# Kernel optimization log

Hardware: AMD Instinct MI355X
Metric: run time of the kernel (lower is better)

The kernel has to match this reference:

```python
import jax, jax.numpy as jnp
import numpy as np

N = 100000   # nodes (single ntype)
R = 3        # relations
E = 500000   # edges per relation
H = 4        # attention heads
F = 64       # out_feat per head
IN = 256     # in_feat
NEG_SLOPE = 0.2  # DGL GATConv default


def setup_inputs() -> dict:
    key = jax.random.key(0)
    ks = jax.random.split(key, 7)
    x = jax.random.normal(ks[0], (N, IN), jnp.float32)
    src = jax.random.randint(ks[1], (R, E), 0, N, dtype=jnp.int32)
    dst = jax.random.randint(ks[2], (R, E), 0, N, dtype=jnp.int32)
    W = jax.random.normal(ks[3], (R, IN, H * F), jnp.float32) / np.sqrt(IN).astype(np.float32)
    attn_l = jax.random.normal(ks[4], (R, H, F), jnp.float32) * 0.1
    attn_r = jax.random.normal(ks[5], (R, H, F), jnp.float32) * 0.1
    bias = jnp.zeros((R, H * F), jnp.float32)
    return {"x": x, "W": W, "attn_l": attn_l, "attn_r": attn_r, "bias": bias,
            "src": src, "dst": dst}


def _gat_relation(x, W_r, al_r, ar_r, b_r, src_r, dst_r):
    # projection: [N, H, F]
    z = (x @ W_r).reshape(N, H, F)
    # per-node attention logits: [N, H]
    el = jnp.sum(z * al_r, axis=-1)
    er = jnp.sum(z * ar_r, axis=-1)
    # edge scores: [E, H]
    e = jax.nn.leaky_relu(el[src_r] + er[dst_r], negative_slope=NEG_SLOPE)
    # segment softmax over incoming edges of each dst node
    m = jax.ops.segment_max(e, dst_r, num_segments=N)      # [N, H]
    ee = jnp.exp(e - m[dst_r])                              # [E, H]
    den = jax.ops.segment_sum(ee, dst_r, num_segments=N)   # [N, H]
    alpha = ee / den[dst_r]                                 # [E, H]
    # weighted scatter-aggregate: [N, H, F]
    rst = jax.ops.segment_sum(z[src_r] * alpha[:, :, None], dst_r, num_segments=N)
    return rst + b_r.reshape(1, H, F)


def reference(x, W, attn_l, attn_r, bias, src, dst):
    # HeteroGraphConv aggregates relations targeting the same ntype with 'sum'
    out = jnp.zeros((N, H, F), x.dtype)
    for r in range(R):
        out = out + _gat_relation(x, W[r], attn_l[r], attn_r[r], bias[r], src[r], dst[r])
    # RelGATConvLayer._apply: activation(h.view(-1, out_feat*num_heads)); dropout=0
    return jax.nn.elu(out.reshape(N, H * F))
```

## Files before the change

### kernel.cpp

```cpp
#include <hip/hip_runtime.h>
#include <hip/hip_bf16.h>


#define RN 100000
#define RE 500000
#define RH 4
#define RIN 256
#define RR 3
#define RHF 256
#define NE3 (RR * RE)
#define N3  (RR * RN)

typedef __attribute__((ext_vector_type(8))) short short8;
typedef __attribute__((ext_vector_type(4))) float f32x4;

static __device__ __forceinline__ float b2f(unsigned short u) {
  return __uint_as_float(((unsigned int)u) << 16);
}
static __device__ __forceinline__ unsigned short f2b(float f) {
  unsigned int u = __float_as_uint(f);
  u += 0x7FFF + ((u >> 16) & 1);
  return (unsigned short)(u >> 16);
}

__global__ __launch_bounds__(256) void rgat_convx(
    const float* __restrict__ x, unsigned short* __restrict__ xb) {
  const size_t i = ((size_t)blockIdx.x * 256 + threadIdx.x) * 4;
  if (i >= (size_t)RN * RIN) return;
  const float4 v = *(const float4*)(x + i);
  ushort4 o;
  o.x = f2b(v.x); o.y = f2b(v.y); o.z = f2b(v.z); o.w = f2b(v.w);
  *(ushort4*)(xb + i) = o;
}

__global__ __launch_bounds__(256) void rgat_convw(
    const float* __restrict__ W, unsigned short* __restrict__ wbt) {
  const int o = blockIdx.x * 256 + threadIdx.x;
  if (o >= RR * RIN * RHF) return;
  const int r = o / (RIN * RHF);
  const int rem = o - r * (RIN * RHF);
  const int n = rem >> 8;
  const int k = rem & 255;
  wbt[o] = f2b(W[r * (RIN * RHF) + k * RHF + n]);
}

__global__ __launch_bounds__(256) void rgat_gemm_bf16(
    const unsigned short* __restrict__ xb, const unsigned short* __restrict__ wbt,
    unsigned short* __restrict__ zb, const float* __restrict__ al,
    const float* __restrict__ ar, float* __restrict__ el,
    float* __restrict__ er) {
  __shared__ unsigned short As[128 * 32];
  __shared__ unsigned short Bs[128 * 32];
  const int tid = threadIdx.x;
  const int lane = tid & 63, wid = tid >> 6;
  const int wr = wid >> 1, wc = wid & 1;
  const int m0 = blockIdx.x * 128;
  const int n0 = blockIdx.y * 128;
  const int r  = blockIdx.z;

  f32x4 acc[4][4] = {};
  const unsigned short* Bbase = wbt + (size_t)r * (RIN * RHF);

  for (int k0 = 0; k0 < RIN; k0 += 32) {
#pragma unroll
    for (int i = 0; i < 2; ++i) {
      const int c = wid * 128 + i * 64 + lane;
      const int row = c >> 2, c4 = c & 3;
      const unsigned short* ga = xb + (size_t)(m0 + row) * RIN + k0 + c4 * 8;
      __builtin_amdgcn_global_load_lds(
          (const __attribute__((address_space(1))) void*)ga,
          (__attribute__((address_space(3))) void*)(As + (wid * 128 + i * 64) * 8),
          16, 0, 0);
      const unsigned short* gb = Bbase + (size_t)(n0 + row) * RIN + k0 + c4 * 8;
      __builtin_amdgcn_global_load_lds(
          (const __attribute__((address_space(1))) void*)gb,
          (__attribute__((address_space(3))) void*)(Bs + (wid * 128 + i * 64) * 8),
          16, 0, 0);
    }
    asm volatile("s_waitcnt vmcnt(0)" ::: "memory");
    __syncthreads();

    short8 af[4], bfr[4];
#pragma unroll
    for (int mi = 0; mi < 4; ++mi)
      af[mi] = *(const short8*)(As + ((wr * 64 + mi * 16 + (lane & 15)) * 32 + (lane >> 4) * 8));
#pragma unroll
    for (int ni = 0; ni < 4; ++ni)
      bfr[ni] = *(const short8*)(Bs + ((wc * 64 + ni * 16 + (lane & 15)) * 32 + (lane >> 4) * 8));
#pragma unroll
    for (int mi = 0; mi < 4; ++mi)
#pragma unroll
      for (int ni = 0; ni < 4; ++ni)
        acc[mi][ni] = __builtin_amdgcn_mfma_f32_16x16x32_bf16(af[mi], bfr[ni], acc[mi][ni], 0, 0, 0);
    __syncthreads();
  }

  const int head = blockIdx.y * 2 + wc;
  float alv[4], arv[4];
#pragma unroll
  for (int ni = 0; ni < 4; ++ni) {
    alv[ni] = al[r * RHF + head * 64 + ni * 16 + (lane & 15)];
    arv[ni] = ar[r * RHF + head * 64 + ni * 16 + (lane & 15)];
  }

  const int mbase = m0 + wr * 64;
#pragma unroll
  for (int mi = 0; mi < 4; ++mi) {
#pragma unroll
    for (int q = 0; q < 4; ++q) {
      const int m = mbase + mi * 16 + (lane >> 4) * 4 + q;
      float pl = 0.f, pr = 0.f;
#pragma unroll
      for (int ni = 0; ni < 4; ++ni) {
        pl += acc[mi][ni][q] * alv[ni];
        pr += acc[mi][ni][q] * arv[ni];
      }
#pragma unroll
      for (int off = 1; off < 16; off <<= 1) {
        pl += __shfl_xor(pl, off);
        pr += __shfl_xor(pr, off);
      }
      if (m < RN) {
        if ((lane & 15) == 0) {
          el[(size_t)(r * (size_t)RN + m) * RH + head] = pl;
          er[(size_t)(r * (size_t)RN + m) * RH + head] = pr;
        }
        unsigned short* zrow = zb + (size_t)r * ((size_t)RN * RHF) + (size_t)m * RHF
                               + n0 + wc * 64 + (lane & 15);
#pragma unroll
        for (int ni = 0; ni < 4; ++ni) zrow[ni * 16] = f2b(acc[mi][ni][q]);
      }
    }
  }
}

__global__ __launch_bounds__(256) void rgat_hist(
    const int* __restrict__ dst, int* __restrict__ deg) {
  const int i = blockIdx.x * 256 + threadIdx.x;
  if (i >= NE3) return;
  const int r = i / RE;
  atomicAdd(&deg[r * RN + dst[i]], 1);
}

__global__ __launch_bounds__(256) void rgat_scan1(
    const int* __restrict__ deg, int* __restrict__ offs, int* __restrict__ bsum) {
  __shared__ int sh[256];
  const int tid = threadIdx.x;
  const int base = blockIdx.x * 1024 + tid * 4;
  int v[4]; int s = 0;
#pragma unroll
  for (int j = 0; j < 4; ++j) {
    v[j] = (base + j < N3) ? deg[base + j] : 0;
    s += v[j];
  }
  sh[tid] = s;
  __syncthreads();
  for (int off = 1; off < 256; off <<= 1) {
    int t = (tid >= off) ? sh[tid - off] : 0;
    __syncthreads();
    sh[tid] += t;
    __syncthreads();
  }
  int run = sh[tid] - s;
  if (tid == 255) bsum[blockIdx.x] = sh[255];
#pragma unroll
  for (int j = 0; j < 4; ++j) {
    if (base + j < N3) offs[base + j] = run;
    run += v[j];
  }
}

__global__ __launch_bounds__(512) void rgat_scan2(int* __restrict__ bsum, int nb) {
  __shared__ int sh[512];
  const int tid = threadIdx.x;
  const int v = (tid < nb) ? bsum[tid] : 0;
  sh[tid] = v;
  __syncthreads();
  for (int off = 1; off < 512; off <<= 1) {
    int t = (tid >= off) ? sh[tid - off] : 0;
    __syncthreads();
    sh[tid] += t;
    __syncthreads();
  }
  if (tid < nb) bsum[tid] = sh[tid] - v;
}

__global__ __launch_bounds__(256) void rgat_scan3(
    int* __restrict__ offs, const int* __restrict__ bsum) {
  const int base = blockIdx.x * 1024 + threadIdx.x * 4;
  const int b = bsum[blockIdx.x];
#pragma unroll
  for (int j = 0; j < 4; ++j)
    if (base + j < N3) offs[base + j] += b;
}

__global__ __launch_bounds__(256) void rgat_scatter(
    const int* __restrict__ src, const int* __restrict__ dst,
    const float* __restrict__ el, const float* __restrict__ er,
    int* __restrict__ offs, int* __restrict__ csr_src,
    float4* __restrict__ csr_ee) {
  const int i = blockIdx.x * 256 + threadIdx.x;
  if (i >= NE3) return;
  const int r = i / RE;
  const int s = src[i];
  const int d = dst[i];
  const int pos = atomicAdd(&offs[r * RN + d], 1);
  const float4 elv = *(const float4*)(el + (size_t)(r * (size_t)RN + s) * RH);
  const float4 erv = *(const float4*)(er + (size_t)(r * (size_t)RN + d) * RH);
  float e0 = elv.x + erv.x, e1 = elv.y + erv.y, e2 = elv.z + erv.z, e3 = elv.w + erv.w;
  e0 = e0 > 0.f ? e0 : 0.2f * e0;
  e1 = e1 > 0.f ? e1 : 0.2f * e1;
  e2 = e2 > 0.f ? e2 : 0.2f * e2;
  e3 = e3 > 0.f ? e3 : 0.2f * e3;
  csr_src[pos] = s;
  csr_ee[pos] = make_float4(__expf(e0), __expf(e1), __expf(e2), __expf(e3));
}

__global__ __launch_bounds__(256) void rgat_aggregate(
    const unsigned short* __restrict__ zb, const int* __restrict__ csr_src,
    const float4* __restrict__ csr_ee, const int* __restrict__ deg,
    const int* __restrict__ offs, const float* __restrict__ bias,
    float* __restrict__ out) {
  __shared__ float sh[3][RHF];
  const int n = blockIdx.x;
  const int wid = threadIdx.x >> 6, lane = threadIdx.x & 63;
  const int h = lane >> 4;
  const int c = lane * 4;

  if (wid < 3) {
    const int r = wid;
    const int base = r * RN + n;
    const int d = deg[base];
    float a0 = 0.f, a1 = 0.f, a2 = 0.f, a3 = 0.f, den = 0.f;
    if (d > 0) {
      const int start = offs[base] - d;
      const unsigned short* zr = zb + (size_t)r * ((size_t)RN * RHF) + c;
      int s = csr_src[start];
      float4 ee = csr_ee[start];
      ushort4 zv = *(const ushort4*)(zr + (size_t)s * RHF);
      for (int e = 0; e < d; ++e) {
        const float a = (h == 0) ? ee.x : (h == 1) ? ee.y : (h == 2) ? ee.z : ee.w;
        const ushort4 zc = zv;
        if (e + 1 < d) {
          s = csr_src[start + e + 1];
          ee = csr_ee[start + e + 1];
          zv = *(const ushort4*)(zr + (size_t)s * RHF);
        }
        a0 += a * b2f(zc.x);
        a1 += a * b2f(zc.y);
        a2 += a * b2f(zc.z);
        a3 += a * b2f(zc.w);
        den += a;
      }
    }
    const float inv = (den > 0.f) ? 1.f / den : 0.f;
    *(float4*)&sh[r][c] = make_float4(a0 * inv, a1 * inv, a2 * inv, a3 * inv);
  }
  __syncthreads();

  const int col = threadIdx.x;
  float v = sh[0][col] + sh[1][col] + sh[2][col]
          + bias[col] + bias[RHF + col] + bias[2 * RHF + col];
  v = v > 0.f ? v : (__expf(v) - 1.f);
  out[(size_t)n * RHF + col] = v;
}

extern "C" void kernel_launch(void* const* d_in, const int* in_sizes, int n_in,
                              void* d_out, int out_size, void* d_ws, size_t ws_size,
                              hipStream_t stream) {
  const float* x    = (const float*)d_in[0];
  const float* W    = (const float*)d_in[1];
  const float* al   = (const float*)d_in[2];
  const float* ar   = (const float*)d_in[3];
  const float* bias = (const float*)d_in[4];
  const int*   src  = (const int*)d_in[5];
  const int*   dst  = (const int*)d_in[6];
  float* out = (float*)d_out;

  char* p = (char*)d_ws;
  unsigned short* xb  = (unsigned short*)p; p += (size_t)RN * RIN * 2;
  unsigned short* wbt = (unsigned short*)p; p += (size_t)RR * RIN * RHF * 2;
  unsigned short* zb  = (unsigned short*)p; p += (size_t)RR * RN * RHF * 2;
  float* el   = (float*)p;  p += (size_t)N3 * RH * 4;
  float* er   = (float*)p;  p += (size_t)N3 * RH * 4;
  int* deg    = (int*)p;    p += (size_t)N3 * 4;
  int* offs   = (int*)p;    p += (size_t)N3 * 4;
  int* csr_s  = (int*)p;    p += (size_t)NE3 * 4;
  float4* csr_ee = (float4*)p; p += (size_t)NE3 * 16;
  int* bsum   = (int*)p;    p += 2048;

  const int NB1 = (N3 + 1023) / 1024;

  hipMemsetAsync(deg, 0, (size_t)N3 * 4, stream);

  rgat_convx<<<(RN * RIN / 4 + 255) / 256, 256, 0, stream>>>(x, xb);
  rgat_convw<<<(RR * RIN * RHF + 255) / 256, 256, 0, stream>>>(W, wbt);

  rgat_hist<<<(NE3 + 255) / 256, 256, 0, stream>>>(dst, deg);
  rgat_scan1<<<NB1, 256, 0, stream>>>(deg, offs, bsum);
  rgat_scan2<<<1, 512, 0, stream>>>(bsum, NB1);
  rgat_scan3<<<NB1, 256, 0, stream>>>(offs, bsum);

  rgat_gemm_bf16<<<dim3((RN + 127) / 128, RHF / 128, RR), 256, 0, stream>>>(
      xb, wbt, zb, al, ar, el, er);

  rgat_scatter<<<(NE3 + 255) / 256, 256, 0, stream>>>(src, dst, el, er, offs,
                                                      csr_s, csr_ee);

  rgat_aggregate<<<RN, 256, 0, stream>>>(zb, csr_s, csr_ee, deg, offs, bias, out);
}
```

Measured before the change: 753.0 us.

## Merge relation CSRs by destination and split edges across all four warps

Builds one CSR keyed only by destination node, merging the three relations, and stores a combined relation-and-source row offset per edge. The aggregate kernel then spreads each node's edges over all four warps in batches of four independent gathers, instead of one warp per relation walking a serial dependent chain with the fourth warp idle. Each edge is routed to a per-relation accumulator by its offset range, and the partial sums and denominators are reduced in shared memory. This shrinks the histogram and scan to N entries and raises memory-level parallelism, at the cost of extra branching per edge and more shared-memory reduction work.

```diff
diff --git a/kernel.cpp b/kernel.cpp
--- a/kernel.cpp
+++ b/kernel.cpp
@@ -9,7 +9,6 @@
 #define RR 3
 #define RHF 256
 #define NE3 (RR * RE)
-#define N3  (RR * RN)
 
 typedef __attribute__((ext_vector_type(8))) short short8;
 typedef __attribute__((ext_vector_type(4))) float f32x4;
@@ -135,11 +134,10 @@
 }
 
 __global__ __launch_bounds__(256) void rgat_hist(
-    const int* __restrict__ dst, int* __restrict__ deg) {
+    const int* __restrict__ dst, int* __restrict__ degm) {
   const int i = blockIdx.x * 256 + threadIdx.x;
   if (i >= NE3) return;
-  const int r = i / RE;
-  atomicAdd(&deg[r * RN + dst[i]], 1);
+  atomicAdd(&degm[dst[i]], 1);
 }
 
 __global__ __launch_bounds__(256) void rgat_scan1(
@@ -150,7 +148,7 @@
   int v[4]; int s = 0;
 #pragma unroll
   for (int j = 0; j < 4; ++j) {
-    v[j] = (base + j < N3) ? deg[base + j] : 0;
+    v[j] = (base + j < RN) ? deg[base + j] : 0;
     s += v[j];
   }
   sh[tid] = s;
@@ -165,7 +163,7 @@
   if (tid == 255) bsum[blockIdx.x] = sh[255];
 #pragma unroll
   for (int j = 0; j < 4; ++j) {
-    if (base + j < N3) offs[base + j] = run;
+    if (base + j < RN) offs[base + j] = run;
     run += v[j];
   }
 }
@@ -191,20 +189,20 @@
   const int b = bsum[blockIdx.x];
 #pragma unroll
   for (int j = 0; j < 4; ++j)
-    if (base + j < N3) offs[base + j] += b;
+    if (base + j < RN) offs[base + j] += b;
 }
 
 __global__ __launch_bounds__(256) void rgat_scatter(
     const int* __restrict__ src, const int* __restrict__ dst,
     const float* __restrict__ el, const float* __restrict__ er,
-    int* __restrict__ offs, int* __restrict__ csr_src,
-    float4* __restrict__ csr_ee) {
+    int* __restrict__ offsm, int* __restrict__ czoff,
+    float4* __restrict__ cee) {
   const int i = blockIdx.x * 256 + threadIdx.x;
   if (i >= NE3) return;
   const int r = i / RE;
   const int s = src[i];
   const int d = dst[i];
-  const int pos = atomicAdd(&offs[r * RN + d], 1);
+  const int pos = atomicAdd(&offsm[d], 1);
   const float4 elv = *(const float4*)(el + (size_t)(r * (size_t)RN + s) * RH);
   const float4 erv = *(const float4*)(er + (size_t)(r * (size_t)RN + d) * RH);
   float e0 = elv.x + erv.x, e1 = elv.y + erv.y, e2 = elv.z + erv.z, e3 = elv.w + erv.w;
@@ -212,55 +210,81 @@
   e1 = e1 > 0.f ? e1 : 0.2f * e1;
   e2 = e2 > 0.f ? e2 : 0.2f * e2;
   e3 = e3 > 0.f ? e3 : 0.2f * e3;
-  csr_src[pos] = s;
-  csr_ee[pos] = make_float4(__expf(e0), __expf(e1), __expf(e2), __expf(e3));
+  czoff[pos] = r * RN + s;
+  cee[pos] = make_float4(__expf(e0), __expf(e1), __expf(e2), __expf(e3));
 }
 
 __global__ __launch_bounds__(256) void rgat_aggregate(
-    const unsigned short* __restrict__ zb, const int* __restrict__ csr_src,
-    const float4* __restrict__ csr_ee, const int* __restrict__ deg,
-    const int* __restrict__ offs, const float* __restrict__ bias,
+    const unsigned short* __restrict__ zb, const int* __restrict__ czoff,
+    const float4* __restrict__ cee, const int* __restrict__ degm,
+    const int* __restrict__ offsm, const float* __restrict__ bias,
     float* __restrict__ out) {
-  __shared__ float sh[3][RHF];
+  __shared__ float shn[4][RR][RHF];
+  __shared__ float shd[4][RR][RH];
   const int n = blockIdx.x;
   const int wid = threadIdx.x >> 6, lane = threadIdx.x & 63;
   const int h = lane >> 4;
   const int c = lane * 4;
 
-  if (wid < 3) {
-    const int r = wid;
-    const int base = r * RN + n;
-    const int d = deg[base];
-    float a0 = 0.f, a1 = 0.f, a2 = 0.f, a3 = 0.f, den = 0.f;
-    if (d > 0) {
-      const int start = offs[base] - d;
-      const unsigned short* zr = zb + (size_t)r * ((size_t)RN * RHF) + c;
-      int s = csr_src[start];
-      float4 ee = csr_ee[start];
-      ushort4 zv = *(const ushort4*)(zr + (size_t)s * RHF);
-      for (int e = 0; e < d; ++e) {
-        const float a = (h == 0) ? ee.x : (h == 1) ? ee.y : (h == 2) ? ee.z : ee.w;
-        const ushort4 zc = zv;
-        if (e + 1 < d) {
-          s = csr_src[start + e + 1];
-          ee = csr_ee[start + e + 1];
-          zv = *(const ushort4*)(zr + (size_t)s * RHF);
-        }
-        a0 += a * b2f(zc.x);
-        a1 += a * b2f(zc.y);
-        a2 += a * b2f(zc.z);
-        a3 += a * b2f(zc.w);
-        den += a;
+  const int d = degm[n];
+  const int start = offsm[n] - d;
+
+  float4 acc0 = {0.f, 0.f, 0.f, 0.f}, acc1 = acc0, acc2 = acc0;
+  float den0 = 0.f, den1 = 0.f, den2 = 0.f;
+
+  const unsigned short* zc = zb + c;
+
+  for (int base = wid; base < d; base += 16) {
+    int zo[4];
+    float4 ef[4];
+    ushort4 zv[4];
+#pragma unroll
+    for (int j = 0; j < 4; ++j) {
+      const int t = base + j * 4;
+      if (t < d) {
+        zo[j] = czoff[start + t];
+        ef[j] = cee[start + t];
+      } else {
+        zo[j] = -1;
       }
     }
-    const float inv = (den > 0.f) ? 1.f / den : 0.f;
-    *(float4*)&sh[r][c] = make_float4(a0 * inv, a1 * inv, a2 * inv, a3 * inv);
+#pragma unroll
+    for (int j = 0; j < 4; ++j)
+      if (zo[j] >= 0) zv[j] = *(const ushort4*)(zc + (size_t)zo[j] * RHF);
+#pragma unroll
+    for (int j = 0; j < 4; ++j) {
+      if (zo[j] < 0) continue;
+      const float a = (h == 0) ? ef[j].x : (h == 1) ? ef[j].y : (h == 2) ? ef[j].z : ef[j].w;
+      const float z0 = b2f(zv[j].x), z1 = b2f(zv[j].y), z2 = b2f(zv[j].z), z3 = b2f(zv[j].w);
+      if (zo[j] < RN) {
+        acc0.x += a * z0; acc0.y += a * z1; acc0.z += a * z2; acc0.w += a * z3; den0 += a;
+      } else if (zo[j] < 2 * RN) {
+        acc1.x += a * z0; acc1.y += a * z1; acc1.z += a * z2; acc1.w += a * z3; den1 += a;
+      } else {
+        acc2.x += a * z0; acc2.y += a * z1; acc2.z += a * z2; acc2.w += a * z3; den2 += a;
+      }
+    }
+  }
+
+  *(float4*)&shn[wid][0][c] = acc0;
+  *(float4*)&shn[wid][1][c] = acc1;
+  *(float4*)&shn[wid][2][c] = acc2;
+  if ((lane & 15) == 0) {
+    shd[wid][0][h] = den0;
+    shd[wid][1][h] = den1;
+    shd[wid][2][h] = den2;
   }
   __syncthreads();
 
   const int col = threadIdx.x;
-  float v = sh[0][col] + sh[1][col] + sh[2][col]
-          + bias[col] + bias[RHF + col] + bias[2 * RHF + col];
+  const int hh = col >> 6;
+  float v = bias[col] + bias[RHF + col] + bias[2 * RHF + col];
+#pragma unroll
+  for (int r = 0; r < RR; ++r) {
+    const float dn = shd[0][r][hh] + shd[1][r][hh] + shd[2][r][hh] + shd[3][r][hh];
+    const float nm = shn[0][r][col] + shn[1][r][col] + shn[2][r][col] + shn[3][r][col];
+    v += (dn > 0.f) ? nm / dn : 0.f;
+  }
   v = v > 0.f ? v : (__expf(v) - 1.f);
   out[(size_t)n * RHF + col] = v;
 }
@@ -281,31 +305,31 @@
   unsigned short* xb  = (unsigned short*)p; p += (size_t)RN * RIN * 2;
   unsigned short* wbt = (unsigned short*)p; p += (size_t)RR * RIN * RHF * 2;
   unsigned short* zb  = (unsigned short*)p; p += (size_t)RR * RN * RHF * 2;
-  float* el   = (float*)p;  p += (size_t)N3 * RH * 4;
-  float* er   = (float*)p;  p += (size_t)N3 * RH * 4;
-  int* deg    = (int*)p;    p += (size_t)N3 * 4;
-  int* offs   = (int*)p;    p += (size_t)N3 * 4;
-  int* csr_s  = (int*)p;    p += (size_t)NE3 * 4;
-  float4* csr_ee = (float4*)p; p += (size_t)NE3 * 16;
-  int* bsum   = (int*)p;    p += 2048;
-
-  const int NB1 = (N3 + 1023) / 1024;
-
-  hipMemsetAsync(deg, 0, (size_t)N3 * 4, stream);
+  float* el    = (float*)p;  p += (size_t)RR * RN * RH * 4;
+  float* er    = (float*)p;  p += (size_t)RR * RN * RH * 4;
+  int* degm    = (int*)p;    p += (size_t)RN * 4;
+  int* offsm   = (int*)p;    p += (size_t)RN * 4;
+  int* czoff   = (int*)p;    p += (size_t)NE3 * 4;
+  float4* cee  = (float4*)p; p += (size_t)NE3 * 16;
+  int* bsum    = (int*)p;    p += 2048;
+
+  const int NB1 = (RN + 1023) / 1024;
+
+  hipMemsetAsync(degm, 0, (size_t)RN * 4, stream);
 
   rgat_convx<<<(RN * RIN / 4 + 255) / 256, 256, 0, stream>>>(x, xb);
   rgat_convw<<<(RR * RIN * RHF + 255) / 256, 256, 0, stream>>>(W, wbt);
 
-  rgat_hist<<<(NE3 + 255) / 256, 256, 0, stream>>>(dst, deg);
-  rgat_scan1<<<NB1, 256, 0, stream>>>(deg, offs, bsum);
+  rgat_hist<<<(NE3 + 255) / 256, 256, 0, stream>>>(dst, degm);
+  rgat_scan1<<<NB1, 256, 0, stream>>>(degm, offsm, bsum);
   rgat_scan2<<<1, 512, 0, stream>>>(bsum, NB1);
-  rgat_scan3<<<NB1, 256, 0, stream>>>(offs, bsum);
+  rgat_scan3<<<NB1, 256, 0, stream>>>(offsm, bsum);
 
   rgat_gemm_bf16<<<dim3((RN + 127) / 128, RHF / 128, RR), 256, 0, stream>>>(
       xb, wbt, zb, al, ar, el, er);
 
-  rgat_scatter<<<(NE3 + 255) / 256, 256, 0, stream>>>(src, dst, el, er, offs,
-                                                      csr_s, csr_ee);
-
-  rgat_aggregate<<<RN, 256, 0, stream>>>(zb, csr_s, csr_ee, deg, offs, bias, out);
-}
+  rgat_scatter<<<(NE3 + 255) / 256, 256, 0, stream>>>(src, dst, el, er, offsm,
+                                                      czoff, cee);
+
+  rgat_aggregate<<<RN, 256, 0, stream>>>(zb, czoff, cee, degm, offsm, bias, out);
+}
```

Result: faster. 646.5 us (-14.1%).
